# Optimization experiments

Hardware: AMD Instinct MI355X
Metric: run time of the kernel (lower is better)

The kernel has to match this reference:

```python
import jax, jax.numpy as jnp
import numpy as np

DIM = 768
HEADS = 12
HEAD_DIM = DIM // HEADS
NUM_CLASSES = 1000
SCALE = HEAD_DIM ** (-0.5)


def setup_inputs() -> dict:
    key = jax.random.key(0)
    ks = jax.random.split(key, 6)
    B, N = 4, 2048
    s = 0.02
    return {
        "x": jax.random.normal(ks[0], (B, N, DIM), dtype=jnp.float32),
        "w_qkv": jax.random.normal(ks[1], (DIM, 3 * DIM), dtype=jnp.float32) * s,
        "w_proj": jax.random.normal(ks[2], (DIM, DIM), dtype=jnp.float32) * s,
        "b_proj": jax.random.normal(ks[3], (DIM,), dtype=jnp.float32) * s,
        "w_head": jax.random.normal(ks[4], (DIM, NUM_CLASSES), dtype=jnp.float32) * s,
        "b_head": jax.random.normal(ks[5], (NUM_CLASSES,), dtype=jnp.float32) * s,
    }


def reference(x, w_qkv, w_proj, b_proj, w_head, b_head):
    B, N, C = x.shape
    qkv = (x @ w_qkv).reshape(B, N, 3, HEADS, HEAD_DIM)
    qkv = jnp.transpose(qkv, (2, 0, 3, 1, 4))  # [3, B, H, N, hd]
    q, k, v = qkv[0], qkv[1], qkv[2]
    attn = jnp.einsum("bhnd,bhmd->bhnm", q, k) * SCALE  # [B,H,N,N]
    attn = jax.nn.softmax(attn, axis=-1)
    out = jnp.einsum("bhnm,bhmd->bhnd", attn, v)  # [B,H,N,hd]
    out = jnp.transpose(out, (0, 2, 1, 3)).reshape(B, N, C)
    out = out @ w_proj + b_proj
    out = out @ w_head + b_head  # [B,N,num_classes]
    return jnp.max(out, axis=1)  # [B,num_classes]
```

## Files before the change

### kernel.cpp

```cpp
#include <hip/hip_runtime.h>
#include <hip/hip_bf16.h>

typedef __attribute__((ext_vector_type(8))) short short8;
typedef __attribute__((ext_vector_type(4))) float f32x4;
typedef __attribute__((ext_vector_type(16))) float f32x16;
typedef unsigned short u16t;
typedef unsigned int u32t;

#define MFMA16(a, b, c) __builtin_amdgcn_mfma_f32_16x16x32_bf16((a), (b), (c), 0, 0, 0)
#define MFMA32(a, b, c) __builtin_amdgcn_mfma_f32_32x32x16_bf16((a), (b), (c), 0, 0, 0)

__device__ __forceinline__ u16t f2b(float f) {
    union { float f; u32t u; } v; v.f = f;
    u32t u = v.u + 0x7FFFu + ((v.u >> 16) & 1u);
    return (u16t)(u >> 16);
}
__device__ __forceinline__ u32t encf(float f) {
    union { float f; u32t u; } v; v.f = f;
    return (v.u & 0x80000000u) ? ~v.u : (v.u | 0x80000000u);
}
__device__ __forceinline__ float decf(u32t u) {
    union { u32t u; float f; } v;
    v.u = (u & 0x80000000u) ? (u ^ 0x80000000u) : ~u;
    return v.f;
}
__device__ __forceinline__ float fexp2(float x) {
#if __has_builtin(__builtin_amdgcn_exp2f)
    return __builtin_amdgcn_exp2f(x);
#else
    return __expf(x * 0.6931471805599453f);
#endif
}
__device__ __forceinline__ void gload16(const u16t* g, u16t* l) {
    __builtin_amdgcn_global_load_lds((const __attribute__((address_space(1))) void*)g,
                                     (__attribute__((address_space(3))) void*)l, 16, 0, 0);
}

__global__ __launch_bounds__(256) void k_cast_x(const float* __restrict__ x, u16t* __restrict__ xb) {
    int i = blockIdx.x * 256 + threadIdx.x;
    float4 v = ((const float4*)x)[i];
    ushort4 o;
    o.x = f2b(v.x); o.y = f2b(v.y); o.z = f2b(v.z); o.w = f2b(v.w);
    ((ushort4*)xb)[i] = o;
}

__global__ __launch_bounds__(256) void k_transpose(const float* __restrict__ W, u16t* __restrict__ WT,
                                                   int K, int N, int NP) {
    __shared__ float t[32][33];
    int n0 = blockIdx.x * 32, k0 = blockIdx.y * 32;
    int tx = threadIdx.x, ty = threadIdx.y;
    for (int i = 0; i < 32; i += 8) {
        int k = k0 + ty + i, n = n0 + tx;
        t[ty + i][tx] = (n < N) ? W[(size_t)k * N + n] : 0.f;
    }
    __syncthreads();
    for (int i = 0; i < 32; i += 8) {
        int n = n0 + ty + i, k = k0 + tx;
        if (n < NP) WT[(size_t)n * K + k] = f2b(t[tx][ty + i]);
    }
}

__global__ __launch_bounds__(256) void k_bias_f(const float* __restrict__ bproj, const float* __restrict__ whead,
                                                const float* __restrict__ bhead, float* __restrict__ bf) {
    __shared__ float red[256];
    int t = threadIdx.x;
    int c = t & 15;
    int jg = t >> 4;
    int n = blockIdx.x * 16 + c;
    float s = 0.f;
    if (n < 1000) {
#pragma unroll 4
        for (int j = jg * 48; j < jg * 48 + 48; ++j)
            s += bproj[j] * whead[j * 1000 + n];
    }
    red[t] = s;
    __syncthreads();
    for (int off = 128; off >= 16; off >>= 1) {
        if (t < off) red[t] += red[t + off];
        __syncthreads();
    }
    if (t < 16) {
        int nn = blockIdx.x * 16 + t;
        bf[nn] = (nn < 1000) ? (red[t] + bhead[nn]) : 0.f;
    }
}

__global__ __launch_bounds__(256) void k_init_out(u32t* __restrict__ o, int n) {
    int i = blockIdx.x * 256 + threadIdx.x;
    if (i < n) o[i] = 0u;
}
__global__ __launch_bounds__(256) void k_decode_out(u32t* __restrict__ o, int n) {
    int i = blockIdx.x * 256 + threadIdx.x;
    if (i < n) {
        float f = decf(o[i]);
        ((float*)o)[i] = f;
    }
}

#define BM 128
#define BN 128

#define QSCALE 0.18033688011112042f

template <int EPI>
__global__ __launch_bounds__(256) void k_gemm_bt(const u16t* __restrict__ A, const u16t* __restrict__ BT,
                                                 int M, int N, int K,
                                                 u16t* __restrict__ Cb, const float* __restrict__ bias,
                                                 u32t* __restrict__ omax) {
    __shared__ alignas(16) u16t As[2][BM * 64];
    __shared__ alignas(16) u16t Bs[2][BN * 64];
    int tid = threadIdx.x;
    int lane = tid & 63, wid = tid >> 6;
    int wr = wid >> 1, wc = wid & 1;
    int g = lane >> 4, l15 = lane & 15;

    int nwg = gridDim.x;
    int bid = blockIdx.x;
    int wg = (bid & 7) * (nwg >> 3) + (bid >> 3);
    int nx = N >> 7;
    int bx = wg % nx, by = wg / nx;
    int m0 = by * BM, n0 = bx * BN;

    f32x4 acc[4][4];
    for (int i = 0; i < 4; i++)
        for (int j = 0; j < 4; j++) acc[i][j] = (f32x4){0.f, 0.f, 0.f, 0.f};

    const u16t* pa[4]; const u16t* pb[4]; u16t* da[4]; u16t* db[4];
#pragma unroll
    for (int i = 0; i < 4; i++) {
        int c = tid + 256 * i;
        int row = (c >> 2) & 127;
        int kcol = (c >> 9) * 32 + (c & 3) * 8;
        pa[i] = A + (size_t)(m0 + row) * K + kcol;
        pb[i] = BT + (size_t)(n0 + row) * K + kcol;
        da[i] = &As[0][c * 8];
        db[i] = &Bs[0][c * 8];
    }

    auto stage = [&](int buf, int k0) {
        int boff = buf * (BM * 64);
#pragma unroll
        for (int i = 0; i < 4; i++) gload16(pa[i] + k0, da[i] + boff);
#pragma unroll
        for (int i = 0; i < 4; i++) gload16(pb[i] + k0, db[i] + boff);
    };

    const int NT = K >> 6;
    stage(0, 0);

#pragma unroll 1
    for (int t = 0; t < NT; ++t) {
        const int cur = t & 1;
        if (t + 1 < NT) {
            stage(cur ^ 1, (t + 1) << 6);
            asm volatile("s_waitcnt vmcnt(8)" ::: "memory");
        } else {
            asm volatile("s_waitcnt vmcnt(0)" ::: "memory");
        }
        __builtin_amdgcn_s_barrier();

        const u16t* Ab = &As[cur][0];
        const u16t* Bb = &Bs[cur][0];
#pragma unroll
        for (int kk = 0; kk < 2; kk++) {
            short8 af[4], bf[4];
#pragma unroll
            for (int i = 0; i < 4; i++) af[i] = *(const short8*)&Ab[kk * 4096 + (wr * 64 + i * 16 + l15) * 32 + g * 8];
#pragma unroll
            for (int j = 0; j < 4; j++) bf[j] = *(const short8*)&Bb[kk * 4096 + (wc * 64 + j * 16 + l15) * 32 + g * 8];
#pragma unroll
            for (int i = 0; i < 4; i++)
#pragma unroll
                for (int j = 0; j < 4; j++) acc[i][j] = MFMA16(af[i], bf[j], acc[i][j]);
        }
        asm volatile("s_waitcnt lgkmcnt(0)" ::: "memory");
        __builtin_amdgcn_s_barrier();
    }

    if constexpr (EPI == 0) {
        for (int i = 0; i < 4; i++)
            for (int j = 0; j < 4; j++)
                for (int r = 0; r < 4; r++) {
                    int row = m0 + wr * 64 + i * 16 + g * 4 + r;
                    int col = n0 + wc * 64 + j * 16 + l15;
                    int t = col / 768, rem = col - t * 768;
                    int hh = rem >> 6, d = rem & 63;
                    int bb = row >> 11, n = row & 2047;
                    float v = acc[i][j][r];
                    size_t idx;
                    if (t == 0) {
                        v *= QSCALE;
                        idx = ((size_t)(bb * 12 + hh)) * 131072 + (size_t)n * 64 + d;
                    } else if (t == 1) {
                        idx = ((size_t)(48 + bb * 12 + hh)) * 131072 + (size_t)n * 64 + d;
                    } else {
                        int np = (n & ~12) | ((n & 4) << 1) | ((n & 8) >> 1);
                        idx = ((size_t)(96 + bb * 12 + hh)) * 131072 + (size_t)d * 2048 + np;
                    }
                    Cb[idx] = f2b(v);
                }
    } else if constexpr (EPI == 1) {
        for (int i = 0; i < 4; i++)
            for (int j = 0; j < 4; j++)
                for (int r = 0; r < 4; r++) {
                    int row = m0 + wr * 64 + i * 16 + g * 4 + r;
                    int col = n0 + wc * 64 + j * 16 + l15;
                    Cb[(size_t)row * N + col] = f2b(acc[i][j][r] + bias[col]);
                }
    } else if constexpr (EPI == 3) {
        for (int i = 0; i < 4; i++)
            for (int j = 0; j < 4; j++)
                for (int r = 0; r < 4; r++) {
                    int row = m0 + wr * 64 + i * 16 + g * 4 + r;
                    int col = n0 + wc * 64 + j * 16 + l15;
                    Cb[(size_t)row * N + col] = f2b(acc[i][j][r]);
                }
    } else {
        __shared__ float smax[2][BN];
        float cmax[4];
        for (int j = 0; j < 4; j++) {
            float m = -3.0e38f;
            for (int i = 0; i < 4; i++)
                for (int r = 0; r < 4; r++) m = fmaxf(m, acc[i][j][r]);
            m = fmaxf(m, __shfl_xor(m, 16));
            m = fmaxf(m, __shfl_xor(m, 32));
            cmax[j] = m;
        }
        __syncthreads();
        if (lane < 16)
            for (int j = 0; j < 4; j++) smax[wr][wc * 64 + j * 16 + lane] = cmax[j];
        __syncthreads();
        if (tid < BN) {
            int col = n0 + tid;
            if (col < 1000) {
                float m = fmaxf(smax[0][tid], smax[1][tid]) + bias[col];
                int b = m0 >> 11;
                atomicMax(&omax[b * 1000 + col], encf(m));
            }
        }
    }
}

__global__ __launch_bounds__(256) void k_flash(const u16t* __restrict__ QKV, u16t* __restrict__ AO) {
    __shared__ alignas(16) u16t Kc[3][4096];
    __shared__ alignas(16) u16t Vc[3][4096];

    const int tid = threadIdx.x;
    const int lane = tid & 63;
    const int h = lane >> 5;
    const int l31 = lane & 31;
    const int w = tid >> 6;
    const int wk = ((blockIdx.x & 7) * 96) + (blockIdx.x >> 3);
    const int qt = wk & 15;
    const int hb = wk >> 4;
    const int head = hb % 12, b = hb / 12;
    const u16t* Qg = QKV + ((size_t)hb) * 131072;
    const u16t* Kg = QKV + ((size_t)(48 + hb)) * 131072;
    const u16t* Vg = QKV + ((size_t)(96 + hb)) * 131072;
    const int q0w = qt * 128 + w * 32;

    short8 qf[4];
#pragma unroll
    for (int ks = 0; ks < 4; ++ks)
        qf[ks] = *(const short8*)&Qg[(size_t)(q0w + l31) * 64 + ks * 16 + h * 8];
    asm volatile("s_waitcnt vmcnt(0)" ::: "memory");

    short8 vone;
#pragma unroll
    for (int e = 0; e < 8; ++e) vone[e] = (short)0x3F80;

    f32x16 o0, o1, lsum;
#pragma unroll
    for (int r = 0; r < 16; ++r) { o0[r] = 0.f; o1[r] = 0.f; lsum[r] = 0.f; }

    auto stage = [&](int bi, int kv0) {
#pragma unroll
        for (int c = 0; c < 2; ++c) {
            int ic = c * 256 + tid;
            int ss = ic >> 8, ks = (ic >> 6) & 3, l6 = ic & 63;
            int hh = l6 >> 5, lq = l6 & 31;
            const u16t* gs = Kg + ((size_t)(kv0 + ss * 32 + lq) << 6) + ks * 16 + hh * 8;
            gload16(gs, &Kc[bi][ic * 8]);
        }
#pragma unroll
        for (int c = 0; c < 2; ++c) {
            int ic = c * 256 + tid;
            int jb = ic >> 8, ks = (ic >> 6) & 3, l6 = ic & 63;
            int hh = l6 >> 5, ld = l6 & 31;
            const u16t* gs = Vg + (size_t)(jb * 32 + ld) * 2048 + kv0 + ks * 16 + hh * 8;
            gload16(gs, &Vc[bi][ic * 8]);
        }
    };

    stage(0, 0);
    stage(1, 64);

#pragma unroll 1
    for (int t = 0; t < 32; ++t) {
        const int cur = t % 3;
        if (t < 30) {
            stage((t + 2) % 3, (t + 2) * 64);
            asm volatile("s_waitcnt vmcnt(8)" ::: "memory");
        } else if (t == 30) {
            asm volatile("s_waitcnt vmcnt(4)" ::: "memory");
        } else {
            asm volatile("s_waitcnt vmcnt(0)" ::: "memory");
        }
        __builtin_amdgcn_s_barrier();

        const u16t* Kb = &Kc[cur][0];
        const u16t* Vb = &Vc[cur][0];

        f32x16 s0, s1;
#pragma unroll
        for (int r = 0; r < 16; ++r) { s0[r] = 0.f; s1[r] = 0.f; }
        __builtin_amdgcn_s_setprio(1);
#pragma unroll
        for (int ks = 0; ks < 4; ++ks) {
            short8 k0 = *(const short8*)&Kb[(ks * 64 + lane) * 8];
            short8 k1 = *(const short8*)&Kb[((4 + ks) * 64 + lane) * 8];
            s0 = MFMA32(k0, qf[ks], s0);
            s1 = MFMA32(k1, qf[ks], s1);
        }
        __builtin_amdgcn_s_setprio(0);

        short8 pf[4];
        auto packhalf = [&](const f32x16& sv, int half, int idx) {
            union { u32t wu[4]; short8 v; } u;
#pragma unroll
            for (int wq = 0; wq < 4; ++wq) {
                float lo = fexp2(sv[half * 8 + 2 * wq]);
                float hi = fexp2(sv[half * 8 + 2 * wq + 1]);
                asm("v_cvt_pk_bf16_f32 %0, %1, %2" : "=v"(u.wu[wq]) : "v"(lo), "v"(hi));
            }
            pf[idx] = u.v;
        };
        packhalf(s0, 0, 0);
        packhalf(s0, 1, 1);
        packhalf(s1, 0, 2);
        packhalf(s1, 1, 3);

        __builtin_amdgcn_s_setprio(1);
#pragma unroll
        for (int ks = 0; ks < 4; ++ks) {
            short8 v0 = *(const short8*)&Vb[(ks * 64 + lane) * 8];
            short8 v1 = *(const short8*)&Vb[((4 + ks) * 64 + lane) * 8];
            o0 = MFMA32(pf[ks], v0, o0);
            o1 = MFMA32(pf[ks], v1, o1);
            lsum = MFMA32(pf[ks], vone, lsum);
        }
        __builtin_amdgcn_s_setprio(0);

        asm volatile("s_waitcnt lgkmcnt(0)" ::: "memory");
        __builtin_amdgcn_s_barrier();
    }

#pragma unroll
    for (int r = 0; r < 16; ++r) {
        int q = (r & 3) + 8 * (r >> 2) + 4 * h;
        float rn = 1.0f / lsum[r];
        u16t* dst = AO + (size_t)(b * 2048 + q0w + q) * 768 + head * 64;
        dst[l31] = f2b(o0[r] * rn);
        dst[32 + l31] = f2b(o1[r] * rn);
    }
}

extern "C" void kernel_launch(void* const* d_in, const int* in_sizes, int n_in,
                              void* d_out, int out_size, void* d_ws, size_t ws_size,
                              hipStream_t stream) {
    const float* x = (const float*)d_in[0];
    const float* w_qkv = (const float*)d_in[1];
    const float* w_proj = (const float*)d_in[2];
    const float* b_proj = (const float*)d_in[3];
    const float* w_head = (const float*)d_in[4];
    const float* b_head = (const float*)d_in[5];

    char* ws = (char*)d_ws;
    u16t* xb = (u16t*)(ws);
    u16t* wqkvT = (u16t*)(ws + 12582912);
    u16t* wheadT = (u16t*)(ws + 16121856);
    u16t* wprojb = (u16t*)(ws + 17694720);
    u16t* qkv = (u16t*)(ws + 18874368);
    u16t* ao = (u16t*)(ws + 56623104);
    u16t* WfT = (u16t*)(ws + 69206016);
    float* bias_f = (float*)(ws + 70778880);

    dim3 tb(32, 8);
    k_cast_x<<<6144, 256, 0, stream>>>(x, xb);
    k_cast_x<<<576, 256, 0, stream>>>(w_proj, (u16t*)wprojb);
    k_transpose<<<dim3(2304 / 32, 768 / 32), tb, 0, stream>>>(w_qkv, wqkvT, 768, 2304, 2304);
    k_transpose<<<dim3(1024 / 32, 768 / 32), tb, 0, stream>>>(w_head, wheadT, 768, 1000, 1024);
    k_init_out<<<16, 256, 0, stream>>>((u32t*)d_out, 4000);
    k_bias_f<<<64, 256, 0, stream>>>(b_proj, w_head, b_head, bias_f);

    k_gemm_bt<3><<<48, 256, 0, stream>>>(wheadT, wprojb, 1024, 768, 768, WfT, nullptr, nullptr);

    k_gemm_bt<0><<<1152, 256, 0, stream>>>(xb, wqkvT, 8192, 2304, 768, qkv, nullptr, nullptr);
    k_flash<<<768, 256, 0, stream>>>(qkv, ao);
    k_gemm_bt<2><<<512, 256, 0, stream>>>(ao, WfT, 8192, 1024, 768, nullptr, bias_f, (u32t*)d_out);

    k_decode_out<<<16, 256, 0, stream>>>((u32t*)d_out, 4000);
}
```

Before: 198.7 us.

## Switch GEMMs to 256x128 tiles with 8 waves and swizzled LDS

The bf16 GEMM kernel now uses 512-thread workgroups (8 waves) computing 256x128 tiles instead of 128x128, halving grid sizes. LDS staging uses an XOR swizzle to reduce bank conflicts, and the next-tile global loads are split into two phases so half are issued between the two k-slices. MFMA sections are also wrapped in s_setprio. The larger tile improves reuse of B, at the cost of more LDS per block and fewer workgroups for the small GEMMs.

```diff
diff --git a/kernel.cpp b/kernel.cpp
--- a/kernel.cpp
+++ b/kernel.cpp
@@ -97,18 +97,19 @@
     }
 }
 
-#define BM 128
+#define BM 256
 #define BN 128
 
 #define QSCALE 0.18033688011112042f
 
 template <int EPI>
-__global__ __launch_bounds__(256) void k_gemm_bt(const u16t* __restrict__ A, const u16t* __restrict__ BT,
-                                                 int M, int N, int K,
-                                                 u16t* __restrict__ Cb, const float* __restrict__ bias,
-                                                 u32t* __restrict__ omax) {
-    __shared__ alignas(16) u16t As[2][BM * 64];
-    __shared__ alignas(16) u16t Bs[2][BN * 64];
+__global__ __launch_bounds__(512, 2) void k_gemm8(const u16t* __restrict__ A, const u16t* __restrict__ BT,
+                                                  int M, int N, int K,
+                                                  u16t* __restrict__ Cb, const float* __restrict__ bias,
+                                                  u32t* __restrict__ omax) {
+    __shared__ alignas(16) u16t Asf[2 * 2 * 8192];
+    __shared__ alignas(16) u16t Bsf[2 * 2 * 4096];
+
     int tid = threadIdx.x;
     int lane = tid & 63, wid = tid >> 6;
     int wr = wid >> 1, wc = wid & 1;
@@ -125,54 +126,92 @@
     for (int i = 0; i < 4; i++)
         for (int j = 0; j < 4; j++) acc[i][j] = (f32x4){0.f, 0.f, 0.f, 0.f};
 
-    const u16t* pa[4]; const u16t* pb[4]; u16t* da[4]; u16t* db[4];
+    const u16t* srcA[4]; u16t* dstA[4];
+#pragma unroll
+    for (int ii = 0; ii < 4; ii++) {
+        int kk = ii >> 1;
+        int cl = wid * 128 + (ii & 1) * 64 + lane;
+        int cd = cl ^ ((cl >> 3) & 3);
+        int arow = cd >> 2, acolc = cd & 3;
+        srcA[ii] = A + (size_t)(m0 + arow) * K + kk * 32 + acolc * 8;
+        dstA[ii] = &Asf[kk * 8192 + cl * 8];
+    }
+    const u16t* srcB[2]; u16t* dstB[2];
+#pragma unroll
+    for (int jj = 0; jj < 2; jj++) {
+        int c = (wid * 2 + jj) * 64 + lane;
+        int kk = c >> 9, cl = c & 511;
+        int cd = cl ^ ((cl >> 3) & 3);
+        srcB[jj] = BT + (size_t)(n0 + (cd >> 2)) * K + kk * 32 + (cd & 3) * 8;
+        dstB[jj] = &Bsf[kk * 4096 + cl * 8];
+    }
+
+    int aoff[4], boff[4];
 #pragma unroll
     for (int i = 0; i < 4; i++) {
-        int c = tid + 256 * i;
-        int row = (c >> 2) & 127;
-        int kcol = (c >> 9) * 32 + (c & 3) * 8;
-        pa[i] = A + (size_t)(m0 + row) * K + kcol;
-        pb[i] = BT + (size_t)(n0 + row) * K + kcol;
-        da[i] = &As[0][c * 8];
-        db[i] = &Bs[0][c * 8];
-    }
-
-    auto stage = [&](int buf, int k0) {
-        int boff = buf * (BM * 64);
-#pragma unroll
-        for (int i = 0; i < 4; i++) gload16(pa[i] + k0, da[i] + boff);
-#pragma unroll
-        for (int i = 0; i < 4; i++) gload16(pb[i] + k0, db[i] + boff);
-    };
+        int lin = ((wr * 64 + i * 16 + l15) << 6) + (g << 4);
+        aoff[i] = (lin ^ (((lin >> 7) & 3) << 4)) >> 1;
+    }
+#pragma unroll
+    for (int j = 0; j < 4; j++) {
+        int lin = ((wc * 64 + j * 16 + l15) << 6) + (g << 4);
+        boff[j] = (lin ^ (((lin >> 7) & 3) << 4)) >> 1;
+    }
+
+#pragma unroll
+    for (int ii = 0; ii < 4; ii++) gload16(srcA[ii], dstA[ii]);
+#pragma unroll
+    for (int jj = 0; jj < 2; jj++) gload16(srcB[jj], dstB[jj]);
 
     const int NT = K >> 6;
-    stage(0, 0);
 
 #pragma unroll 1
     for (int t = 0; t < NT; ++t) {
-        const int cur = t & 1;
+        const int d = t & 1, nd = d ^ 1;
         if (t + 1 < NT) {
-            stage(cur ^ 1, (t + 1) << 6);
-            asm volatile("s_waitcnt vmcnt(8)" ::: "memory");
+            int ko = (t + 1) << 6;
+            gload16(srcA[0] + ko, dstA[0] + nd * 16384);
+            gload16(srcA[1] + ko, dstA[1] + nd * 16384);
+            gload16(srcB[0] + ko, dstB[0] + nd * 8192);
+            gload16(srcB[1] + ko, dstB[1] + nd * 8192);
+            asm volatile("s_waitcnt vmcnt(4)" ::: "memory");
         } else {
             asm volatile("s_waitcnt vmcnt(0)" ::: "memory");
         }
         __builtin_amdgcn_s_barrier();
 
-        const u16t* Ab = &As[cur][0];
-        const u16t* Bb = &Bs[cur][0];
-#pragma unroll
-        for (int kk = 0; kk < 2; kk++) {
-            short8 af[4], bf[4];
-#pragma unroll
-            for (int i = 0; i < 4; i++) af[i] = *(const short8*)&Ab[kk * 4096 + (wr * 64 + i * 16 + l15) * 32 + g * 8];
-#pragma unroll
-            for (int j = 0; j < 4; j++) bf[j] = *(const short8*)&Bb[kk * 4096 + (wc * 64 + j * 16 + l15) * 32 + g * 8];
-#pragma unroll
-            for (int i = 0; i < 4; i++)
-#pragma unroll
-                for (int j = 0; j < 4; j++) acc[i][j] = MFMA16(af[i], bf[j], acc[i][j]);
-        }
+        const u16t* Ab = &Asf[d * 16384];
+        const u16t* Bb = &Bsf[d * 8192];
+
+        short8 af[4], bf[4];
+#pragma unroll
+        for (int i = 0; i < 4; i++) af[i] = *(const short8*)&Ab[aoff[i]];
+#pragma unroll
+        for (int j = 0; j < 4; j++) bf[j] = *(const short8*)&Bb[boff[j]];
+        __builtin_amdgcn_s_setprio(1);
+#pragma unroll
+        for (int i = 0; i < 4; i++)
+#pragma unroll
+            for (int j = 0; j < 4; j++) acc[i][j] = MFMA16(af[i], bf[j], acc[i][j]);
+        __builtin_amdgcn_s_setprio(0);
+
+        if (t + 1 < NT) {
+            int ko = (t + 1) << 6;
+            gload16(srcA[2] + ko, dstA[2] + nd * 16384);
+            gload16(srcA[3] + ko, dstA[3] + nd * 16384);
+        }
+
+#pragma unroll
+        for (int i = 0; i < 4; i++) af[i] = *(const short8*)&Ab[8192 + aoff[i]];
+#pragma unroll
+        for (int j = 0; j < 4; j++) bf[j] = *(const short8*)&Bb[4096 + boff[j]];
+        __builtin_amdgcn_s_setprio(1);
+#pragma unroll
+        for (int i = 0; i < 4; i++)
+#pragma unroll
+            for (int j = 0; j < 4; j++) acc[i][j] = MFMA16(af[i], bf[j], acc[i][j]);
+        __builtin_amdgcn_s_setprio(0);
+
         asm volatile("s_waitcnt lgkmcnt(0)" ::: "memory");
         __builtin_amdgcn_s_barrier();
     }
@@ -199,14 +238,6 @@
                     }
                     Cb[idx] = f2b(v);
                 }
-    } else if constexpr (EPI == 1) {
-        for (int i = 0; i < 4; i++)
-            for (int j = 0; j < 4; j++)
-                for (int r = 0; r < 4; r++) {
-                    int row = m0 + wr * 64 + i * 16 + g * 4 + r;
-                    int col = n0 + wc * 64 + j * 16 + l15;
-                    Cb[(size_t)row * N + col] = f2b(acc[i][j][r] + bias[col]);
-                }
     } else if constexpr (EPI == 3) {
         for (int i = 0; i < 4; i++)
             for (int j = 0; j < 4; j++)
@@ -216,7 +247,7 @@
                     Cb[(size_t)row * N + col] = f2b(acc[i][j][r]);
                 }
     } else {
-        __shared__ float smax[2][BN];
+        __shared__ float smax[4][BN];
         float cmax[4];
         for (int j = 0; j < 4; j++) {
             float m = -3.0e38f;
@@ -233,7 +264,8 @@
         if (tid < BN) {
             int col = n0 + tid;
             if (col < 1000) {
-                float m = fmaxf(smax[0][tid], smax[1][tid]) + bias[col];
+                float m = fmaxf(fmaxf(smax[0][tid], smax[1][tid]),
+                                fmaxf(smax[2][tid], smax[3][tid])) + bias[col];
                 int b = m0 >> 11;
                 atomicMax(&omax[b * 1000 + col], encf(m));
             }
@@ -393,11 +425,11 @@
     k_init_out<<<16, 256, 0, stream>>>((u32t*)d_out, 4000);
     k_bias_f<<<64, 256, 0, stream>>>(b_proj, w_head, b_head, bias_f);
 
-    k_gemm_bt<3><<<48, 256, 0, stream>>>(wheadT, wprojb, 1024, 768, 768, WfT, nullptr, nullptr);
-
-    k_gemm_bt<0><<<1152, 256, 0, stream>>>(xb, wqkvT, 8192, 2304, 768, qkv, nullptr, nullptr);
+    k_gemm8<3><<<24, 512, 0, stream>>>(wheadT, wprojb, 1024, 768, 768, WfT, nullptr, nullptr);
+
+    k_gemm8<0><<<576, 512, 0, stream>>>(xb, wqkvT, 8192, 2304, 768, qkv, nullptr, nullptr);
     k_flash<<<768, 256, 0, stream>>>(qkv, ao);
-    k_gemm_bt<2><<<512, 256, 0, stream>>>(ao, WfT, 8192, 1024, 768, nullptr, bias_f, (u32t*)d_out);
+    k_gemm8<2><<<256, 512, 0, stream>>>(ao, WfT, 8192, 1024, 768, nullptr, bias_f, (u32t*)d_out);
 
     k_decode_out<<<16, 256, 0, stream>>>((u32t*)d_out, 4000);
 }
```

Measured after the change: 213.2 us. +7.3%, slower.

## Merge small prep kernels and independent GEMMs into combined launches

Applied to the files above, without the earlier changes.

Folds the two cast kernels into one launch and the two transposes into one. The QKV GEMM, the folded head-weight GEMM, the bias fold and the output init now run as block-range branches of a single mega kernel. This cuts the launch count from eleven to six and lets the small independent jobs fill the GPU alongside the big GEMM instead of running serially. The cost is that every block of the mega kernel reserves the full GEMM shared memory, and the small-job blocks run after the large GEMM blocks in launch order.

```diff
diff --git a/kernel.cpp b/kernel.cpp
--- a/kernel.cpp
+++ b/kernel.cpp
@@ -36,18 +36,27 @@
                                      (__attribute__((address_space(3))) void*)l, 16, 0, 0);
 }
 
-__global__ __launch_bounds__(256) void k_cast_x(const float* __restrict__ x, u16t* __restrict__ xb) {
-    int i = blockIdx.x * 256 + threadIdx.x;
-    float4 v = ((const float4*)x)[i];
+__global__ __launch_bounds__(256) void k_cast2(const float* __restrict__ x, u16t* __restrict__ xb,
+                                               const float* __restrict__ wp, u16t* __restrict__ wpb) {
+    int b = blockIdx.x;
+    const float* src; u16t* dst; int i;
+    if (b < 6144) { src = x;  dst = xb;  i = b * 256 + threadIdx.x; }
+    else          { src = wp; dst = wpb; i = (b - 6144) * 256 + threadIdx.x; }
+    float4 v = ((const float4*)src)[i];
     ushort4 o;
     o.x = f2b(v.x); o.y = f2b(v.y); o.z = f2b(v.z); o.w = f2b(v.w);
-    ((ushort4*)xb)[i] = o;
-}
-
-__global__ __launch_bounds__(256) void k_transpose(const float* __restrict__ W, u16t* __restrict__ WT,
-                                                   int K, int N, int NP) {
+    ((ushort4*)dst)[i] = o;
+}
+
+__global__ __launch_bounds__(256) void k_transpose2(const float* __restrict__ Wq, u16t* __restrict__ WqT,
+                                                    const float* __restrict__ Wh, u16t* __restrict__ WhT) {
     __shared__ float t[32][33];
-    int n0 = blockIdx.x * 32, k0 = blockIdx.y * 32;
+    int bxr = blockIdx.x;
+    const float* W; u16t* WT; int N, NP, n0;
+    if (bxr < 72) { W = Wq; WT = WqT; N = 2304; NP = 2304; n0 = bxr * 32; }
+    else          { W = Wh; WT = WhT; N = 1000; NP = 1024; n0 = (bxr - 72) * 32; }
+    const int K = 768;
+    int k0 = blockIdx.y * 32;
     int tx = threadIdx.x, ty = threadIdx.y;
     for (int i = 0; i < 32; i += 8) {
         int k = k0 + ty + i, n = n0 + tx;
@@ -60,35 +69,6 @@
     }
 }
 
-__global__ __launch_bounds__(256) void k_bias_f(const float* __restrict__ bproj, const float* __restrict__ whead,
-                                                const float* __restrict__ bhead, float* __restrict__ bf) {
-    __shared__ float red[256];
-    int t = threadIdx.x;
-    int c = t & 15;
-    int jg = t >> 4;
-    int n = blockIdx.x * 16 + c;
-    float s = 0.f;
-    if (n < 1000) {
-#pragma unroll 4
-        for (int j = jg * 48; j < jg * 48 + 48; ++j)
-            s += bproj[j] * whead[j * 1000 + n];
-    }
-    red[t] = s;
-    __syncthreads();
-    for (int off = 128; off >= 16; off >>= 1) {
-        if (t < off) red[t] += red[t + off];
-        __syncthreads();
-    }
-    if (t < 16) {
-        int nn = blockIdx.x * 16 + t;
-        bf[nn] = (nn < 1000) ? (red[t] + bhead[nn]) : 0.f;
-    }
-}
-
-__global__ __launch_bounds__(256) void k_init_out(u32t* __restrict__ o, int n) {
-    int i = blockIdx.x * 256 + threadIdx.x;
-    if (i < n) o[i] = 0u;
-}
 __global__ __launch_bounds__(256) void k_decode_out(u32t* __restrict__ o, int n) {
     int i = blockIdx.x * 256 + threadIdx.x;
     if (i < n) {
@@ -103,20 +83,16 @@
 #define QSCALE 0.18033688011112042f
 
 template <int EPI>
-__global__ __launch_bounds__(256) void k_gemm_bt(const u16t* __restrict__ A, const u16t* __restrict__ BT,
-                                                 int M, int N, int K,
-                                                 u16t* __restrict__ Cb, const float* __restrict__ bias,
-                                                 u32t* __restrict__ omax) {
-    __shared__ alignas(16) u16t As[2][BM * 64];
-    __shared__ alignas(16) u16t Bs[2][BN * 64];
+__device__ __forceinline__ void gemm_core(u16t* As, u16t* Bs,
+                                          const u16t* __restrict__ A, const u16t* __restrict__ BT,
+                                          int M, int N, int K,
+                                          u16t* __restrict__ Cb, const float* __restrict__ bias,
+                                          u32t* __restrict__ omax, int wg) {
     int tid = threadIdx.x;
     int lane = tid & 63, wid = tid >> 6;
     int wr = wid >> 1, wc = wid & 1;
     int g = lane >> 4, l15 = lane & 15;
 
-    int nwg = gridDim.x;
-    int bid = blockIdx.x;
-    int wg = (bid & 7) * (nwg >> 3) + (bid >> 3);
     int nx = N >> 7;
     int bx = wg % nx, by = wg / nx;
     int m0 = by * BM, n0 = bx * BN;
@@ -133,8 +109,8 @@
         int kcol = (c >> 9) * 32 + (c & 3) * 8;
         pa[i] = A + (size_t)(m0 + row) * K + kcol;
         pb[i] = BT + (size_t)(n0 + row) * K + kcol;
-        da[i] = &As[0][c * 8];
-        db[i] = &Bs[0][c * 8];
+        da[i] = &As[c * 8];
+        db[i] = &Bs[c * 8];
     }
 
     auto stage = [&](int buf, int k0) {
@@ -159,8 +135,8 @@
         }
         __builtin_amdgcn_s_barrier();
 
-        const u16t* Ab = &As[cur][0];
-        const u16t* Bb = &Bs[cur][0];
+        const u16t* Ab = &As[cur * (BM * 64)];
+        const u16t* Bb = &Bs[cur * (BN * 64)];
 #pragma unroll
         for (int kk = 0; kk < 2; kk++) {
             short8 af[4], bf[4];
@@ -199,14 +175,6 @@
                     }
                     Cb[idx] = f2b(v);
                 }
-    } else if constexpr (EPI == 1) {
-        for (int i = 0; i < 4; i++)
-            for (int j = 0; j < 4; j++)
-                for (int r = 0; r < 4; r++) {
-                    int row = m0 + wr * 64 + i * 16 + g * 4 + r;
-                    int col = n0 + wc * 64 + j * 16 + l15;
-                    Cb[(size_t)row * N + col] = f2b(acc[i][j][r] + bias[col]);
-                }
     } else if constexpr (EPI == 3) {
         for (int i = 0; i < 4; i++)
             for (int j = 0; j < 4; j++)
@@ -216,7 +184,7 @@
                     Cb[(size_t)row * N + col] = f2b(acc[i][j][r]);
                 }
     } else {
-        __shared__ float smax[2][BN];
+        float* smax = (float*)As;
         float cmax[4];
         for (int j = 0; j < 4; j++) {
             float m = -3.0e38f;
@@ -228,17 +196,72 @@
         }
         __syncthreads();
         if (lane < 16)
-            for (int j = 0; j < 4; j++) smax[wr][wc * 64 + j * 16 + lane] = cmax[j];
+            for (int j = 0; j < 4; j++) smax[wr * BN + wc * 64 + j * 16 + lane] = cmax[j];
         __syncthreads();
         if (tid < BN) {
             int col = n0 + tid;
             if (col < 1000) {
-                float m = fmaxf(smax[0][tid], smax[1][tid]) + bias[col];
+                float m = fmaxf(smax[tid], smax[BN + tid]) + bias[col];
                 int b = m0 >> 11;
                 atomicMax(&omax[b * 1000 + col], encf(m));
             }
         }
     }
+}
+
+__global__ __launch_bounds__(256) void k_mega(const u16t* __restrict__ xb, const u16t* __restrict__ wqkvT,
+                                              u16t* __restrict__ qkv,
+                                              const u16t* __restrict__ wheadT, const u16t* __restrict__ wprojb,
+                                              u16t* __restrict__ WfT,
+                                              const float* __restrict__ bproj, const float* __restrict__ whead,
+                                              const float* __restrict__ bhead, float* __restrict__ bias_f,
+                                              u32t* __restrict__ outb) {
+    __shared__ alignas(16) u16t As[2 * BM * 64];
+    __shared__ alignas(16) u16t Bs[2 * BN * 64];
+    int bid = blockIdx.x;
+    if (bid < 1152) {
+        int wg = (bid & 7) * 144 + (bid >> 3);
+        gemm_core<0>(As, Bs, xb, wqkvT, 8192, 2304, 768, qkv, nullptr, nullptr, wg);
+    } else if (bid < 1200) {
+        int q = bid - 1152;
+        int wg = (q & 7) * 6 + (q >> 3);
+        gemm_core<3>(As, Bs, wheadT, wprojb, 1024, 768, 768, WfT, nullptr, nullptr, wg);
+    } else if (bid < 1264) {
+        float* red = (float*)As;
+        int t = threadIdx.x;
+        int c = t & 15;
+        int jg = t >> 4;
+        int blk = bid - 1200;
+        int n = blk * 16 + c;
+        float s = 0.f;
+        if (n < 1000) {
+#pragma unroll 4
+            for (int j = jg * 48; j < jg * 48 + 48; ++j)
+                s += bproj[j] * whead[j * 1000 + n];
+        }
+        red[t] = s;
+        __syncthreads();
+        for (int off = 128; off >= 16; off >>= 1) {
+            if (t < off) red[t] += red[t + off];
+            __syncthreads();
+        }
+        if (t < 16) {
+            int nn = blk * 16 + t;
+            bias_f[nn] = (nn < 1000) ? (red[t] + bhead[nn]) : 0.f;
+        }
+    } else {
+        int i = (bid - 1264) * 256 + threadIdx.x;
+        if (i < 4000) outb[i] = 0u;
+    }
+}
+
+__global__ __launch_bounds__(256) void k_gemm_fin(const u16t* __restrict__ A, const u16t* __restrict__ BT,
+                                                  const float* __restrict__ bias, u32t* __restrict__ omax) {
+    __shared__ alignas(16) u16t As[2 * BM * 64];
+    __shared__ alignas(16) u16t Bs[2 * BN * 64];
+    int bid = blockIdx.x;
+    int wg = (bid & 7) * 64 + (bid >> 3);
+    gemm_core<2>(As, Bs, A, BT, 8192, 1024, 768, nullptr, bias, omax, wg);
 }
 
 __global__ __launch_bounds__(256) void k_flash(const u16t* __restrict__ QKV, u16t* __restrict__ AO) {
@@ -386,18 +409,11 @@
     float* bias_f = (float*)(ws + 70778880);
 
     dim3 tb(32, 8);
-    k_cast_x<<<6144, 256, 0, stream>>>(x, xb);
-    k_cast_x<<<576, 256, 0, stream>>>(w_proj, (u16t*)wprojb);
-    k_transpose<<<dim3(2304 / 32, 768 / 32), tb, 0, stream>>>(w_qkv, wqkvT, 768, 2304, 2304);
-    k_transpose<<<dim3(1024 / 32, 768 / 32), tb, 0, stream>>>(w_head, wheadT, 768, 1000, 1024);
-    k_init_out<<<16, 256, 0, stream>>>((u32t*)d_out, 4000);
-    k_bias_f<<<64, 256, 0, stream>>>(b_proj, w_head, b_head, bias_f);
-
-    k_gemm_bt<3><<<48, 256, 0, stream>>>(wheadT, wprojb, 1024, 768, 768, WfT, nullptr, nullptr);
-
-    k_gemm_bt<0><<<1152, 256, 0, stream>>>(xb, wqkvT, 8192, 2304, 768, qkv, nullptr, nullptr);
+    k_cast2<<<6720, 256, 0, stream>>>(x, xb, w_proj, wprojb);
+    k_transpose2<<<dim3(104, 24), tb, 0, stream>>>(w_qkv, wqkvT, w_head, wheadT);
+    k_mega<<<1280, 256, 0, stream>>>(xb, wqkvT, qkv, wheadT, wprojb, WfT,
+                                     b_proj, w_head, b_head, bias_f, (u32t*)d_out);
     k_flash<<<768, 256, 0, stream>>>(qkv, ao);
-    k_gemm_bt<2><<<512, 256, 0, stream>>>(ao, WfT, 8192, 1024, 768, nullptr, bias_f, (u32t*)d_out);
-
+    k_gemm_fin<<<512, 256, 0, stream>>>(ao, WfT, bias_f, (u32t*)d_out);
     k_decode_out<<<16, 256, 0, stream>>>((u32t*)d_out, 4000);
 }
```

New measurement: 173.1 us. -12.9%, faster.
